# Optimization experiments

Hardware: AMD Instinct MI355X
Metric: run time of the kernel (lower is better)

## Reference

```python
import jax, jax.numpy as jnp
import numpy as np

B, S, P, D = 32, 512, 512, 768

def setup_inputs() -> dict:
    key = jax.random.key(0)
    k1, k2 = jax.random.split(key)
    inputs = jax.random.normal(k1, (B, S, D), dtype=jnp.float32)
    prototypes = jax.random.normal(k2, (P, D), dtype=jnp.float32)
    return {"inputs": inputs, "prototypes": prototypes}

def reference(inputs, prototypes):
    # Squared Euclidean distance from every token vector to every prototype:
    # but the cross term is a GEMM and the huge [B,S,P,D] intermediate is never built).
    x_sq = jnp.sum(inputs * inputs, axis=-1, keepdims=True)          # [B, S, 1]
    p_sq = jnp.sum(prototypes * prototypes, axis=-1)                 # [P]
    cross = jnp.einsum('bsd,pd->bsp', inputs, prototypes)            # [B, S, P]
    distances = x_sq + p_sq[None, None, :] - 2.0 * cross             # [B, S, P]
    return (distances, prototypes)
```

## Files before the change

### kernel.cpp

```cpp
#include <hip/hip_runtime.h>
#include <hip/hip_bf16.h>


#define M_TOK 16384
#define N_PROT 512
#define K_DIM 768
#define BK 32
#define NCH (K_DIM / BK)
#define APAD 8

typedef __attribute__((ext_vector_type(4))) float f32x4;
typedef __attribute__((ext_vector_type(8))) short bf16x8;

typedef const __attribute__((address_space(1))) unsigned int g_uint;
typedef __attribute__((address_space(3))) unsigned int l_uint;

__device__ inline unsigned short f2bf(float f) {
    unsigned int u = __float_as_uint(f);
    u += 0x7fffu + ((u >> 16) & 1u);
    return (unsigned short)(u >> 16);
}

__global__ __launch_bounds__(256) void prep_b(
    const float* __restrict__ p,
    unsigned short* __restrict__ b_bf, float* __restrict__ p_sq,
    float* __restrict__ proto_out)
{
    const int row  = blockIdx.x * 4 + (threadIdx.x >> 6);
    const int lane = threadIdx.x & 63;

    const float4* src4 = (const float4*)(p + (size_t)row * K_DIM);
    unsigned short* dst = b_bf + (size_t)row * K_DIM;
    float4* pout4 = (float4*)(proto_out + (size_t)row * K_DIM);

    float ssum = 0.0f;
#pragma unroll
    for (int j = 0; j < 3; ++j) {
        const int idx = lane + j * 64;
        float4 v = src4[idx];
        ssum += v.x * v.x + v.y * v.y + v.z * v.z + v.w * v.w;
        ushort4 b;
        b.x = f2bf(v.x); b.y = f2bf(v.y); b.z = f2bf(v.z); b.w = f2bf(v.w);
        ((ushort4*)dst)[idx] = b;
        pout4[idx] = v;
    }
#pragma unroll
    for (int off = 32; off > 0; off >>= 1) ssum += __shfl_down(ssum, off);
    if (lane == 0) p_sq[row] = ssum;
}

__global__ __launch_bounds__(512, 2) void dist_main(
    const float* __restrict__ X,
    const unsigned short* __restrict__ Bb,
    const float* __restrict__ p_sq,
    float* __restrict__ out)
{
    __shared__ unsigned short lds_b[N_PROT * BK];
    __shared__ unsigned short lds_a[64 * (BK + APAD)];
    __shared__ float lds_xsq[64];

    const int tid  = threadIdx.x;
    const int wave = tid >> 6;
    const int lane = tid & 63;
    const int bm   = blockIdx.x << 6;
    const int wn   = wave << 6;
    const int quad = lane >> 4;
    const int l16  = lane & 15;

    const int arow  = tid >> 3;
    const int acol8 = tid & 7;
    const float* aptr = X + (size_t)(bm + arow) * K_DIM + acol8 * 4;

    const int brow = (lane >> 2);
    const int bcol = (lane & 3) * 8;

    const f32x4 zero = {0.0f, 0.0f, 0.0f, 0.0f};
    f32x4 acc[4][4];
#pragma unroll
    for (int mt = 0; mt < 4; ++mt)
#pragma unroll
        for (int nt = 0; nt < 4; ++nt) acc[mt][nt] = zero;

    float asq = 0.0f;
    f32x4 cur = *(const f32x4*)aptr;

    for (int kc = 0; kc < NCH; ++kc) {
        const int k0 = kc * BK;

        __syncthreads();

#pragma unroll
        for (int j = 0; j < 4; ++j) {
            const unsigned short* gb = Bb
                + (size_t)(wn + j * 16 + brow) * K_DIM + k0 + bcol;
            __builtin_amdgcn_global_load_lds((g_uint*)gb,
                (l_uint*)&lds_b[(wn + j * 16) * BK], 16, 0, 0);
        }

        f32x4 nxt = cur;
        if (kc + 1 < NCH)
            nxt = *(const f32x4*)(aptr + k0 + BK);
        asq += cur.x * cur.x + cur.y * cur.y + cur.z * cur.z + cur.w * cur.w;
        ushort4 ua;
        ua.x = f2bf(cur.x); ua.y = f2bf(cur.y);
        ua.z = f2bf(cur.z); ua.w = f2bf(cur.w);
        *(ushort4*)&lds_a[arow * (BK + APAD) + acol8 * 4] = ua;
        cur = nxt;

        __syncthreads();

        bf16x8 af[4], bfr[4];
#pragma unroll
        for (int mt = 0; mt < 4; ++mt)
            af[mt] = *(const bf16x8*)
                &lds_a[(mt * 16 + l16) * (BK + APAD) + quad * 8];
#pragma unroll
        for (int nt = 0; nt < 4; ++nt)
            bfr[nt] = *(const bf16x8*)
                &lds_b[(wn + nt * 16 + l16) * BK + quad * 8];

#pragma unroll
        for (int mt = 0; mt < 4; ++mt)
#pragma unroll
            for (int nt = 0; nt < 4; ++nt)
                acc[mt][nt] = __builtin_amdgcn_mfma_f32_16x16x32_bf16(
                    af[mt], bfr[nt], acc[mt][nt], 0, 0, 0);
    }

#pragma unroll
    for (int off = 1; off < 8; off <<= 1) asq += __shfl_xor(asq, off);
    if (acol8 == 0) lds_xsq[arow] = asq;
    __syncthreads();

    float ps[4];
#pragma unroll
    for (int nt = 0; nt < 4; ++nt) ps[nt] = p_sq[wn + nt * 16 + l16];

#pragma unroll
    for (int mt = 0; mt < 4; ++mt) {
#pragma unroll
        for (int i = 0; i < 4; ++i) {
            const int lr = mt * 16 + quad * 4 + i;
            const float xs = lds_xsq[lr];
            float* orow = out + (size_t)(bm + lr) * N_PROT + wn + l16;
#pragma unroll
            for (int nt = 0; nt < 4; ++nt)
                orow[nt * 16] = xs + ps[nt] - 2.0f * acc[mt][nt][i];
        }
    }
}

extern "C" void kernel_launch(void* const* d_in, const int* in_sizes, int n_in,
                              void* d_out, int out_size, void* d_ws, size_t ws_size,
                              hipStream_t stream) {
    const float* inputs = (const float*)d_in[0];
    const float* protos = (const float*)d_in[1];
    float* out = (float*)d_out;
    float* proto_out = out + (size_t)M_TOK * N_PROT;

    char* ws = (char*)d_ws;
    unsigned short* b_bf = (unsigned short*)ws;
    float* p_sq = (float*)(ws + 786432);

    prep_b<<<128, 256, 0, stream>>>(protos, b_bf, p_sq, proto_out);
    dist_main<<<M_TOK / 64, 512, 0, stream>>>(inputs, b_bf, p_sq, out);
}
```

Measured before the change: 121.8 us.

## Stage full A tile in LDS once and load B fragments directly from global

The kernel now converts the block's entire 64x768 row tile of inputs to bf16 in LDS up front, computing the row norms there. Inside the K loop it drops all __syncthreads. B fragments are read straight from global memory into registers with one-chunk register prefetching, replacing the async global-to-LDS copies. The intent is to remove per-iteration barriers and the LDS round trip for B. In exchange, LDS use grows to about 99KB per block, which may limit occupancy relative to the requested two blocks per CU. B reads are also uncoalesced 16-byte loads per lane that rely on L2 and caches.

```diff
diff --git a/kernel.cpp b/kernel.cpp
--- a/kernel.cpp
+++ b/kernel.cpp
@@ -7,13 +7,10 @@
 #define K_DIM 768
 #define BK 32
 #define NCH (K_DIM / BK)
-#define APAD 8
+#define ASTR (K_DIM + 8)
 
 typedef __attribute__((ext_vector_type(4))) float f32x4;
 typedef __attribute__((ext_vector_type(8))) short bf16x8;
-
-typedef const __attribute__((address_space(1))) unsigned int g_uint;
-typedef __attribute__((address_space(3))) unsigned int l_uint;
 
 __device__ inline unsigned short f2bf(float f) {
     unsigned int u = __float_as_uint(f);
@@ -55,8 +52,7 @@
     const float* __restrict__ p_sq,
     float* __restrict__ out)
 {
-    __shared__ unsigned short lds_b[N_PROT * BK];
-    __shared__ unsigned short lds_a[64 * (BK + APAD)];
+    __shared__ unsigned short lds_a[64 * ASTR];
     __shared__ float lds_xsq[64];
 
     const int tid  = threadIdx.x;
@@ -67,12 +63,24 @@
     const int quad = lane >> 4;
     const int l16  = lane & 15;
 
-    const int arow  = tid >> 3;
-    const int acol8 = tid & 7;
-    const float* aptr = X + (size_t)(bm + arow) * K_DIM + acol8 * 4;
+    const int ar = tid >> 3;
+    const int ac = tid & 7;
+    const float* aptr = X + (size_t)(bm + ar) * K_DIM;
+    float asq = 0.0f;
+#pragma unroll
+    for (int j = 0; j < 24; ++j) {
+        const int c4 = ac + 8 * j;
+        float4 v = *(const float4*)(aptr + (size_t)c4 * 4);
+        asq += v.x * v.x + v.y * v.y + v.z * v.z + v.w * v.w;
+        ushort4 u;
+        u.x = f2bf(v.x); u.y = f2bf(v.y); u.z = f2bf(v.z); u.w = f2bf(v.w);
+        *(ushort4*)&lds_a[ar * ASTR + c4 * 4] = u;
+    }
+#pragma unroll
+    for (int off = 1; off < 8; off <<= 1) asq += __shfl_xor(asq, off);
+    if (ac == 0) lds_xsq[ar] = asq;
 
-    const int brow = (lane >> 2);
-    const int bcol = (lane & 3) * 8;
+    __syncthreads();
 
     const f32x4 zero = {0.0f, 0.0f, 0.0f, 0.0f};
     f32x4 acc[4][4];
@@ -81,56 +89,36 @@
 #pragma unroll
         for (int nt = 0; nt < 4; ++nt) acc[mt][nt] = zero;
 
-    float asq = 0.0f;
-    f32x4 cur = *(const f32x4*)aptr;
+    const unsigned short* bp = Bb + (size_t)(wn + l16) * K_DIM + quad * 8;
+
+    bf16x8 bcur[4], bnxt[4];
+#pragma unroll
+    for (int nt = 0; nt < 4; ++nt)
+        bcur[nt] = *(const bf16x8*)(bp + (size_t)(nt * 16) * K_DIM);
 
     for (int kc = 0; kc < NCH; ++kc) {
         const int k0 = kc * BK;
-
-        __syncthreads();
-
+        if (kc + 1 < NCH) {
 #pragma unroll
-        for (int j = 0; j < 4; ++j) {
-            const unsigned short* gb = Bb
-                + (size_t)(wn + j * 16 + brow) * K_DIM + k0 + bcol;
-            __builtin_amdgcn_global_load_lds((g_uint*)gb,
-                (l_uint*)&lds_b[(wn + j * 16) * BK], 16, 0, 0);
+            for (int nt = 0; nt < 4; ++nt)
+                bnxt[nt] = *(const bf16x8*)(bp + (size_t)(nt * 16) * K_DIM + k0 + BK);
         }
 
-        f32x4 nxt = cur;
-        if (kc + 1 < NCH)
-            nxt = *(const f32x4*)(aptr + k0 + BK);
-        asq += cur.x * cur.x + cur.y * cur.y + cur.z * cur.z + cur.w * cur.w;
-        ushort4 ua;
-        ua.x = f2bf(cur.x); ua.y = f2bf(cur.y);
-        ua.z = f2bf(cur.z); ua.w = f2bf(cur.w);
-        *(ushort4*)&lds_a[arow * (BK + APAD) + acol8 * 4] = ua;
-        cur = nxt;
-
-        __syncthreads();
-
-        bf16x8 af[4], bfr[4];
+        bf16x8 af[4];
 #pragma unroll
         for (int mt = 0; mt < 4; ++mt)
-            af[mt] = *(const bf16x8*)
-                &lds_a[(mt * 16 + l16) * (BK + APAD) + quad * 8];
-#pragma unroll
-        for (int nt = 0; nt < 4; ++nt)
-            bfr[nt] = *(const bf16x8*)
-                &lds_b[(wn + nt * 16 + l16) * BK + quad * 8];
+            af[mt] = *(const bf16x8*)&lds_a[(mt * 16 + l16) * ASTR + k0 + quad * 8];
 
 #pragma unroll
         for (int mt = 0; mt < 4; ++mt)
 #pragma unroll
             for (int nt = 0; nt < 4; ++nt)
                 acc[mt][nt] = __builtin_amdgcn_mfma_f32_16x16x32_bf16(
-                    af[mt], bfr[nt], acc[mt][nt], 0, 0, 0);
-    }
+                    af[mt], bcur[nt], acc[mt][nt], 0, 0, 0);
 
 #pragma unroll
-    for (int off = 1; off < 8; off <<= 1) asq += __shfl_xor(asq, off);
-    if (acol8 == 0) lds_xsq[arow] = asq;
-    __syncthreads();
+        for (int nt = 0; nt < 4; ++nt) bcur[nt] = bnxt[nt];
+    }
 
     float ps[4];
 #pragma unroll
```

Result: faster. 116.1 us (-4.7%).
